# Kernel optimization log

Hardware: AMD Instinct MI355X
Metric: run time of the kernel (lower is better)

## Reference

```python
import jax, jax.numpy as jnp
import numpy as np

B, N, C, H = 4, 4096, 128, 4


def setup_inputs() -> dict:
    key = jax.random.key(0)
    ks = jax.random.split(key, 12)
    def rn(k, shape, s=0.02):
        return jax.random.normal(k, shape, jnp.float32) * s
    return dict(
        x=jax.random.normal(ks[0], (B, N, C), jnp.float32),
        p=jax.random.normal(ks[1], (B, N, 3), jnp.float32),
        fcl1_w=rn(ks[2], (C, C)), fcl1_b=jnp.zeros((C,), jnp.float32),
        # per-head (stacked over leading H axis) TransformerLayer params
        hq_w=rn(ks[3], (H, C, C)), hq_b=jnp.zeros((H, C), jnp.float32),
        hk_w=rn(ks[4], (H, C, C)), hk_b=jnp.zeros((H, C), jnp.float32),
        hv_w=rn(ks[5], (H, C, C)), hv_b=jnp.zeros((H, C), jnp.float32),
        pe1_w=rn(ks[6], (H, C, 3)), pe1_b=jnp.zeros((H, C), jnp.float32),  # Conv1d(3->C, k=1)
        pe2_w=rn(ks[7], (H, C, C)), pe2_b=jnp.zeros((H, C), jnp.float32),  # Conv1d(C->C, k=1)
        mh_w=rn(ks[8], (C, 4 * C)), mh_b=jnp.zeros((C,), jnp.float32),
        fcl2_w=rn(ks[9], (C, C)), fcl2_b=jnp.zeros((C,), jnp.float32),
    )


def reference(x, p, fcl1_w, fcl1_b, hq_w, hq_b, hk_w, hk_b, hv_w, hv_b,
              pe1_w, pe1_b, pe2_w, pe2_b, mh_w, mh_b, fcl2_w, fcl2_b):
    residual = x
    xf = x @ fcl1_w.T + fcl1_b  # fcl1
    scale = 1.0 / jnp.sqrt(jnp.asarray(C, jnp.float32))

    def head(qw, qb, kw, kb, vw, vb, p1w, p1b, p2w, p2b):
        # kernel-size-1 Conv1d == pointwise linear over coords
        pe = jax.nn.relu(jnp.einsum('bnd,cd->bnc', p, p1w) + p1b)
        pe = jnp.einsum('bnc,dc->bnd', pe, p2w) + p2b
        xh = xf + pe
        q = xh @ kw.T + kb  # note: original uses self.key for x_query
        k = xh @ qw.T + qb  # and self.query for x_key (name swap, kept faithful)
        v = xh @ vw.T + vb
        s = jax.nn.softmax(jnp.einsum('bnc,bmc->bnm', q, k) * scale, axis=-1)
        return jnp.einsum('bnm,bmc->bnc', s, v)

    outs = jax.vmap(head)(hq_w, hq_b, hk_w, hk_b, hv_w, hv_b,
                          pe1_w, pe1_b, pe2_w, pe2_b)  # [H,B,N,C]
    cat = jnp.moveaxis(outs, 0, 2).reshape(B, N, H * C)  # concat head1..head4 on last dim
    y = cat @ mh_w.T + mh_b
    y = y @ fcl2_w.T + fcl2_b
    mu = jnp.mean(y, axis=-1, keepdims=True)
    var = jnp.var(y, axis=-1, keepdims=True)
    y = (y - mu) / jnp.sqrt(var + 1e-5)  # torch.layer_norm, no affine
    return (y + residual, p)
```

## Files before the change

kernel.cpp:

```cpp
#include <hip/hip_runtime.h>
#include <hip/hip_bf16.h>

typedef __bf16 bf16;
typedef bf16 bf16x8 __attribute__((ext_vector_type(8)));
typedef float f32x4 __attribute__((ext_vector_type(4)));

static __device__ __forceinline__ f32x4 mfma16(bf16x8 a, bf16x8 b, f32x4 c) {
  return __builtin_amdgcn_mfma_f32_16x16x32_bf16(a, b, c, 0, 0, 0);
}

#define N_SEG 18
#define TOTAL_CONV 2511616

__global__ void probe_k(const unsigned short* __restrict__ xr, int* __restrict__ flag) {
  int wild = 0;
#pragma unroll
  for (int i = 0; i < 8; i++) {
    unsigned short w = xr[threadIdx.x * 8 + i];
    int e = (w >> 7) & 0xFF;
    if (e < 110 || e > 134) wild++;
  }
#pragma unroll
  for (int off = 1; off < 64; off <<= 1) wild += __shfl_xor(wild, off);
  if (threadIdx.x == 0) *flag = (wild > 64) ? 1 : 0;
}

struct ConvArgs { const void* src[N_SEG]; };

__global__ __launch_bounds__(256) void convall_k(ConvArgs a, bf16* __restrict__ dst,
                                                 void* __restrict__ outp,
                                                 const int* __restrict__ flag) {
  const int ends[N_SEG] = {2097152, 2146304, 2162688, 2162816, 2228352, 2228864,
                           2294400, 2294912, 2360448, 2360960, 2362496, 2363008,
                           2428544, 2429056, 2494592, 2495104, 2511488, 2511616};
  int i = blockIdx.x * 256 + threadIdx.x;
  if (i >= TOTAL_CONV) {
    int j = i - TOTAL_CONV;
    if (j < 49152) {
      if (*flag) ((float*)outp)[2097152 + j] = ((const float*)a.src[1])[j];
      else       ((bf16*)outp)[2097152 + j]  = ((const bf16*)a.src[1])[j];
    }
    return;
  }
  int s = 0;
  while (i >= ends[s]) s++;
  int j = i - (s ? ends[s - 1] : 0);
  if (*flag) dst[i] = (bf16)((const float*)a.src[s])[j];
  else       dst[i] = ((const bf16*)a.src[s])[j];
}

__global__ __launch_bounds__(256, 2) void pre_k(
    const bf16* __restrict__ x, const bf16* __restrict__ p,
    const bf16* __restrict__ f1w, const bf16* __restrict__ f1b,
    const bf16* __restrict__ pe1w, const bf16* __restrict__ pe1b,
    const bf16* __restrict__ pe2w, const bf16* __restrict__ pe2b,
    const bf16* __restrict__ Wq, const bf16* __restrict__ Bq,
    const bf16* __restrict__ Wk, const bf16* __restrict__ Bk,
    const bf16* __restrict__ Wv, const bf16* __restrict__ Bv,
    bf16* __restrict__ qo, bf16* __restrict__ ko, bf16* __restrict__ vo)
{
  const int lane = threadIdx.x & 63;
  const int wave = threadIdx.x >> 6;
  const int quad = lane >> 4;
  const int n15 = lane & 15;
  const int h = blockIdx.y;
  const int r0 = blockIdx.x * 64;
  const int wr = wave * 16;

  __shared__ bf16 tile[9216];

  f32x4 acc[8];
  const f32x4 zz = {};

  {
    bf16x8 ap = {};
    if (quad == 0) {
      const bf16* pr = p + (long)(r0 + wr + n15) * 3;
      ap[0] = pr[0]; ap[1] = pr[1]; ap[2] = pr[2];
    }
#pragma unroll
    for (int ct = 0; ct < 8; ct++) {
      bf16x8 bw = {};
      if (quad == 0) {
        const bf16* wp = pe1w + ((long)h * 128 + ct * 16 + n15) * 3;
        bw[0] = wp[0]; bw[1] = wp[1]; bw[2] = wp[2];
      }
      acc[ct] = mfma16(ap, bw, zz);
    }
#pragma unroll
    for (int ct = 0; ct < 8; ct++) {
      const int col = ct * 16 + n15;
      const float bb = (float)pe1b[h * 128 + col];
#pragma unroll
      for (int r = 0; r < 4; r++)
        tile[(wr + quad * 4 + r) * 136 + col] = (bf16)fmaxf(acc[ct][r] + bb, 0.f);
    }
  }

#pragma unroll
  for (int ct = 0; ct < 8; ct++) acc[ct] = zz;
#pragma unroll
  for (int kk = 0; kk < 4; kk++) {
    const int ka = kk * 32 + quad * 8;
    bf16x8 a0 = *(const bf16x8*)&tile[(wr + n15) * 136 + ka];
#pragma unroll
    for (int ct = 0; ct < 8; ct++) {
      bf16x8 wf = *(const bf16x8*)(pe2w + (long)h * 16384 + (long)(ct * 16 + n15) * 128 + ka);
      acc[ct] = mfma16(a0, wf, acc[ct]);
    }
  }
#pragma unroll
  for (int kk = 0; kk < 4; kk++) {
    const int ka = kk * 32 + quad * 8;
    bf16x8 a0 = *(const bf16x8*)(x + (long)(r0 + wr + n15) * 128 + ka);
#pragma unroll
    for (int ct = 0; ct < 8; ct++) {
      bf16x8 wf = *(const bf16x8*)(f1w + (long)(ct * 16 + n15) * 128 + ka);
      acc[ct] = mfma16(a0, wf, acc[ct]);
    }
  }
#pragma unroll
  for (int ct = 0; ct < 8; ct++) {
    const int col = ct * 16 + n15;
    const float bv = (float)pe2b[h * 128 + col] + (float)f1b[col];
#pragma unroll
    for (int r = 0; r < 4; r++)
      tile[(wr + quad * 4 + r) * 136 + col] = (bf16)(acc[ct][r] + bv);
  }

  bf16x8 af[4];
#pragma unroll
  for (int kk = 0; kk < 4; kk++)
    af[kk] = *(const bf16x8*)&tile[(wr + n15) * 136 + kk * 32 + quad * 8];

#pragma unroll
  for (int m = 0; m < 2; m++) {
    f32x4 a2[8];
#pragma unroll
    for (int ct = 0; ct < 8; ct++) a2[ct] = zz;
    const bf16* Wm = (m == 0) ? Wq : Wk;
#pragma unroll
    for (int kk = 0; kk < 4; kk++) {
      const int ka = kk * 32 + quad * 8;
#pragma unroll
      for (int ct = 0; ct < 8; ct++) {
        bf16x8 wf = *(const bf16x8*)(Wm + (long)h * 16384 + (long)(ct * 16 + n15) * 128 + ka);
        a2[ct] = mfma16(af[kk], wf, a2[ct]);
      }
    }
    bf16* oz = ((m == 0) ? qo : ko) + (long)h * 2097152;
    const bf16* Bz = (m == 0) ? Bq : Bk;
#pragma unroll
    for (int ct = 0; ct < 8; ct++) {
      const int col = ct * 16 + n15;
      const float bv = (float)Bz[h * 128 + col];
#pragma unroll
      for (int r = 0; r < 4; r++)
        oz[(long)(r0 + wr + quad * 4 + r) * 128 + col] = (bf16)(a2[ct][r] + bv);
    }
  }

  {
    f32x4 a2[8];
#pragma unroll
    for (int ct = 0; ct < 8; ct++) a2[ct] = zz;
#pragma unroll
    for (int kk = 0; kk < 4; kk++) {
      const int ka = kk * 32 + quad * 8;
#pragma unroll
      for (int ct = 0; ct < 8; ct++) {
        bf16x8 wf = *(const bf16x8*)(Wv + (long)h * 16384 + (long)(ct * 16 + n15) * 128 + ka);
        a2[ct] = mfma16(af[kk], wf, a2[ct]);
      }
    }
    __syncthreads();
#pragma unroll
    for (int ct = 0; ct < 8; ct++) {
      const int col = ct * 16 + n15;
      const float bv = (float)Bv[h * 128 + col];
#pragma unroll
      for (int r = 0; r < 4; r++)
        tile[col * 72 + (wr + quad * 4 + r)] = (bf16)(a2[ct][r] + bv);
    }
    __syncthreads();
    bf16* vz = vo + (long)h * 2097152;
#pragma unroll
    for (int i = 0; i < 16; i++) {
      const int c = wave * 32 + i * 2 + (lane >> 5);
      const int m2 = (lane & 31) * 2;
      *(unsigned int*)&vz[(long)c * 16384 + r0 + m2] =
          *(const unsigned int*)&tile[c * 72 + m2];
    }
  }
}

__global__ __launch_bounds__(256, 2) void attn_k(
    const bf16* __restrict__ Q, const bf16* __restrict__ Kg,
    const bf16* __restrict__ vT, bf16* __restrict__ Op, float* __restrict__ ls)
{
  const int lane = threadIdx.x & 63;
  const int wave = threadIdx.x >> 6;
  const int quad = lane >> 4;
  const int n15 = lane & 15;
  const int qt = blockIdx.x >> 1;
  const int half = blockIdx.x & 1;
  const int b = blockIdx.y, h = blockIdx.z;
  const long qkBase = ((long)h * 4 + b) * 4096 * 128;
  const long vBase = (long)h * (128L * 16384) + (long)b * 4096;
  const int wrow = qt * 128 + wave * 32;
  const int kvStart = half * 2048;

  __shared__ bf16 Kt[64 * 128];
  __shared__ bf16 Vt[128 * 64];
  __shared__ bf16 Pt[4][1024];

  const float scale = 0.08838834764831845f;
  bf16x8 qf[2][4];
#pragma unroll
  for (int g = 0; g < 2; g++)
#pragma unroll
    for (int kk = 0; kk < 4; kk++) {
      bf16x8 t = *(const bf16x8*)(Q + qkBase + (long)(wrow + g * 16 + n15) * 128 + kk * 32 + quad * 8);
#pragma unroll
      for (int j = 0; j < 8; j++) t[j] = (bf16)((float)t[j] * scale);
      qf[g][kk] = t;
    }

  f32x4 Om[2][8] = {};
  float l_part[2][4] = {};

  for (int kv0 = kvStart; kv0 < kvStart + 2048; kv0 += 64) {
    __syncthreads();
    {
      const int rr = threadIdx.x >> 4;
      const int ch = threadIdx.x & 15;
#pragma unroll
      for (int i = 0; i < 4; i++) {
        const int row = rr + i * 16;
        *(bf16x8*)&Kt[row * 128 + ((ch ^ rr) * 8)] =
            *(const bf16x8*)(Kg + qkBase + (long)(kv0 + row) * 128 + ch * 8);
      }
      const int vc = threadIdx.x >> 3;
      const int vch = threadIdx.x & 7;
#pragma unroll
      for (int i = 0; i < 4; i++) {
        const int c = vc + i * 32;
        *(bf16x8*)&Vt[c * 64 + ((vch ^ (c & 7)) * 8)] =
            *(const bf16x8*)(vT + vBase + (long)c * 16384 + kv0 + vch * 8);
      }
    }
    __syncthreads();

    f32x4 S[2][4] = {};
#pragma unroll
    for (int kk = 0; kk < 4; kk++) {
#pragma unroll
      for (int ct = 0; ct < 4; ct++) {
        bf16x8 kf = *(const bf16x8*)&Kt[(ct * 16 + n15) * 128 + (((kk * 4 + quad) ^ n15) * 8)];
        S[0][ct] = mfma16(qf[0][kk], kf, S[0][ct]);
        S[1][ct] = mfma16(qf[1][kk], kf, S[1][ct]);
      }
    }

    bf16x8 pf[2][2];
#pragma unroll
    for (int g = 0; g < 2; g++) {
#pragma unroll
      for (int ct = 0; ct < 4; ct++)
#pragma unroll
        for (int r = 0; r < 4; r++) {
          float e = __expf(S[g][ct][r]);
          l_part[g][r] += e;
          const int row = quad * 4 + r;
          const int kv = ct * 16 + n15;
          Pt[wave][row * 64 + ((((kv >> 3) ^ (row & 7)) * 8)) + (kv & 7)] = (bf16)e;
        }
#pragma unroll
      for (int kk = 0; kk < 2; kk++)
        pf[g][kk] = *(const bf16x8*)&Pt[wave][n15 * 64 + (((kk * 4 + quad) ^ (n15 & 7)) * 8)];
    }

#pragma unroll
    for (int kk = 0; kk < 2; kk++) {
      bf16x8 vf[8];
#pragma unroll
      for (int ct = 0; ct < 8; ct++) {
        const int c = ct * 16 + n15;
        vf[ct] = *(const bf16x8*)&Vt[c * 64 + (((kk * 4 + quad) ^ (c & 7)) * 8)];
      }
#pragma unroll
      for (int g = 0; g < 2; g++)
#pragma unroll
        for (int ct = 0; ct < 8; ct++)
          Om[g][ct] = mfma16(pf[g][kk], vf[ct], Om[g][ct]);
    }
  }

#pragma unroll
  for (int g = 0; g < 2; g++) {
#pragma unroll
    for (int r = 0; r < 4; r++) {
      float s = l_part[g][r];
#pragma unroll
      for (int off = 1; off < 16; off <<= 1) s += __shfl_xor(s, off);
      if (n15 == 0)
        ls[((long)half * 4 + h) * 16384 + b * 4096 + wrow + g * 16 + quad * 4 + r] = s;
    }
    const long ob = (long)half * 8388608 + (long)(b * 4096 + wrow + g * 16 + quad * 4) * 512 + h * 128;
#pragma unroll
    for (int ct = 0; ct < 8; ct++)
#pragma unroll
      for (int r = 0; r < 4; r++)
        Op[ob + (long)r * 512 + ct * 16 + n15] = (bf16)Om[g][ct][r];
  }
}

__global__ __launch_bounds__(256) void tail_k(
    const bf16* __restrict__ Op, const float* __restrict__ ls,
    const bf16* __restrict__ mhw, const bf16* __restrict__ mhb,
    const bf16* __restrict__ f2w, const bf16* __restrict__ f2b,
    const void* __restrict__ xraw, void* __restrict__ outraw,
    const int* __restrict__ flag)
{
  const int lane = threadIdx.x & 63;
  const int wave = threadIdx.x >> 6;
  const int quad = lane >> 4;
  const int n15 = lane & 15;
  const int r0 = blockIdx.x * 64 + wave * 16;
  __shared__ bf16 y1t[64][136];

  float invA[4];
#pragma unroll
  for (int hh = 0; hh < 4; hh++) {
    const float l0 = ls[(long)hh * 16384 + r0 + n15];
    const float l1 = ls[(long)(4 + hh) * 16384 + r0 + n15];
    invA[hh] = 1.f / (l0 + l1);
  }

  f32x4 acc[8] = {};
  for (int k0 = 0; k0 < 512; k0 += 32) {
    const int hh = k0 >> 7;
    const int ka = k0 + quad * 8;
    bf16x8 v0 = *(const bf16x8*)(Op + (long)(r0 + n15) * 512 + ka);
    bf16x8 v1 = *(const bf16x8*)(Op + 8388608L + (long)(r0 + n15) * 512 + ka);
    bf16x8 a0;
#pragma unroll
    for (int j = 0; j < 8; j++)
      a0[j] = (bf16)(((float)v0[j] + (float)v1[j]) * invA[hh]);
#pragma unroll
    for (int ct = 0; ct < 8; ct++) {
      bf16x8 wf = *(const bf16x8*)(mhw + (long)(ct * 16 + n15) * 512 + ka);
      acc[ct] = mfma16(a0, wf, acc[ct]);
    }
  }
#pragma unroll
  for (int ct = 0; ct < 8; ct++) {
    const float bv = (float)mhb[ct * 16 + n15];
#pragma unroll
    for (int r = 0; r < 4; r++)
      y1t[wave * 16 + quad * 4 + r][ct * 16 + n15] = (bf16)(acc[ct][r] + bv);
  }

  f32x4 acc2[8] = {};
  for (int k0 = 0; k0 < 128; k0 += 32) {
    const int ka = k0 + quad * 8;
    bf16x8 a0 = *(const bf16x8*)&y1t[wave * 16 + n15][ka];
#pragma unroll
    for (int ct = 0; ct < 8; ct++) {
      bf16x8 wf = *(const bf16x8*)(f2w + (long)(ct * 16 + n15) * 128 + ka);
      acc2[ct] = mfma16(a0, wf, acc2[ct]);
    }
  }

  float s1[4] = {}, s2[4] = {};
#pragma unroll
  for (int ct = 0; ct < 8; ct++) {
    const float bv = (float)f2b[ct * 16 + n15];
#pragma unroll
    for (int r = 0; r < 4; r++) {
      const float v = acc2[ct][r] + bv;
      acc2[ct][r] = v;
      s1[r] += v;
      s2[r] += v * v;
    }
  }
  float mu[4], inv[4];
#pragma unroll
  for (int r = 0; r < 4; r++) {
    float a = s1[r], b2 = s2[r];
#pragma unroll
    for (int off = 1; off < 16; off <<= 1) {
      a += __shfl_xor(a, off);
      b2 += __shfl_xor(b2, off);
    }
    mu[r] = a * (1.f / 128.f);
    const float var = fmaxf(b2 * (1.f / 128.f) - mu[r] * mu[r], 0.f);
    inv[r] = rsqrtf(var + 1e-5f);
  }

  const int isF32 = *flag;
#pragma unroll
  for (int ct = 0; ct < 8; ct++)
#pragma unroll
    for (int r = 0; r < 4; r++) {
      const long idx = (long)(r0 + quad * 4 + r) * 128 + ct * 16 + n15;
      const float resid = isF32 ? ((const float*)xraw)[idx]
                                : (float)((const bf16*)xraw)[idx];
      const float v = (acc2[ct][r] - mu[r]) * inv[r] + resid;
      if (isF32) ((float*)outraw)[idx] = v;
      else       ((bf16*)outraw)[idx] = (bf16)v;
    }
}

extern "C" void kernel_launch(void* const* d_in, const int* in_sizes, int n_in,
                              void* d_out, int out_size, void* d_ws, size_t ws_size,
                              hipStream_t stream)
{
  bf16* ws  = (bf16*)d_ws;
  bf16* q   = ws;
  bf16* kb  = ws + 8388608;
  bf16* vt  = ws + 16777216;
  bf16* Op  = ws + 25165824;
  float* lsb = (float*)(ws + 41943040);
  const long AR = 42205184;
  int* flag = (int*)(ws + 44720000);

  static const int counts[N_SEG] = {2097152, 49152, 16384, 128, 65536, 512, 65536, 512,
                                    65536, 512, 1536, 512, 65536, 512, 65536, 512, 16384, 128};
  long offs[N_SEG]; long o = AR;
  for (int i = 0; i < N_SEG; i++) { offs[i] = o; o += counts[i]; }
  bf16* xc    = ws + offs[0];
  bf16* pc    = ws + offs[1];
  bf16* f1w   = ws + offs[2];
  bf16* f1b   = ws + offs[3];
  bf16* hqw   = ws + offs[4];
  bf16* hqb   = ws + offs[5];
  bf16* hkw   = ws + offs[6];
  bf16* hkb   = ws + offs[7];
  bf16* hvw   = ws + offs[8];
  bf16* hvb   = ws + offs[9];
  bf16* pe1w  = ws + offs[10];
  bf16* pe1b  = ws + offs[11];
  bf16* pe2w  = ws + offs[12];
  bf16* pe2b  = ws + offs[13];
  bf16* mhw   = ws + offs[14];
  bf16* mhb   = ws + offs[15];
  bf16* f2w   = ws + offs[16];
  bf16* f2b   = ws + offs[17];

  probe_k<<<dim3(1), dim3(64), 0, stream>>>((const unsigned short*)d_in[0], flag);
  ConvArgs ca;
  for (int i = 0; i < N_SEG; i++) ca.src[i] = d_in[i];
  convall_k<<<dim3((TOTAL_CONV + 49152 + 255) / 256), dim3(256), 0, stream>>>(ca, ws + AR, d_out, flag);

  dim3 blk(256);
  pre_k<<<dim3(256, 4), blk, 0, stream>>>(xc, pc, f1w, f1b, pe1w, pe1b, pe2w, pe2b,
                                          hkw, hkb, hqw, hqb, hvw, hvb, q, kb, vt);
  attn_k<<<dim3(64, 4, 4), blk, 0, stream>>>(q, kb, vt, Op, lsb);
  tail_k<<<dim3(256), blk, 0, stream>>>(Op, lsb, mhw, mhb, f2w, f2b, d_in[0], d_out, flag);
}
```

Baseline: 368.9 us.

## Fold softmax scale into Q projection and stream Q fragments from global in attention loop

Moves the 1/sqrt(C) scale into the Q projection epilogue so the attention kernel no longer rescales Q. The attention kernel stops holding the Q fragments in registers and reloads them from global memory (through the cache) on every KV tile. It also gives each 16-row group its own P buffer in shared memory so P fragments are loaded just before their use. The aim is to cut register pressure, which may help occupancy under launch_bounds(256,2), at the cost of repeated global Q loads and doubled Pt shared memory.

```diff
diff --git a/kernel.cpp b/kernel.cpp
--- a/kernel.cpp
+++ b/kernel.cpp
@@ -150,13 +150,14 @@
     }
     bf16* oz = ((m == 0) ? qo : ko) + (long)h * 2097152;
     const bf16* Bz = (m == 0) ? Bq : Bk;
+    const float sc = (m == 0) ? 0.08838834764831845f : 1.0f;
 #pragma unroll
     for (int ct = 0; ct < 8; ct++) {
       const int col = ct * 16 + n15;
       const float bv = (float)Bz[h * 128 + col];
 #pragma unroll
       for (int r = 0; r < 4; r++)
-        oz[(long)(r0 + wr + quad * 4 + r) * 128 + col] = (bf16)(a2[ct][r] + bv);
+        oz[(long)(r0 + wr + quad * 4 + r) * 128 + col] = (bf16)((a2[ct][r] + bv) * sc);
     }
   }
 
@@ -212,19 +213,9 @@
 
   __shared__ bf16 Kt[64 * 128];
   __shared__ bf16 Vt[128 * 64];
-  __shared__ bf16 Pt[4][1024];
-
-  const float scale = 0.08838834764831845f;
-  bf16x8 qf[2][4];
-#pragma unroll
-  for (int g = 0; g < 2; g++)
-#pragma unroll
-    for (int kk = 0; kk < 4; kk++) {
-      bf16x8 t = *(const bf16x8*)(Q + qkBase + (long)(wrow + g * 16 + n15) * 128 + kk * 32 + quad * 8);
-#pragma unroll
-      for (int j = 0; j < 8; j++) t[j] = (bf16)((float)t[j] * scale);
-      qf[g][kk] = t;
-    }
+  __shared__ bf16 Pt[8][1024];
+
+  const bf16* qrow = Q + qkBase + (long)(wrow + n15) * 128 + quad * 8;
 
   f32x4 Om[2][8] = {};
   float l_part[2][4] = {};
@@ -254,17 +245,18 @@
     f32x4 S[2][4] = {};
 #pragma unroll
     for (int kk = 0; kk < 4; kk++) {
+      bf16x8 q0 = *(const bf16x8*)(qrow + kk * 32);
+      bf16x8 q1 = *(const bf16x8*)(qrow + 2048 + kk * 32);
 #pragma unroll
       for (int ct = 0; ct < 4; ct++) {
         bf16x8 kf = *(const bf16x8*)&Kt[(ct * 16 + n15) * 128 + (((kk * 4 + quad) ^ n15) * 8)];
-        S[0][ct] = mfma16(qf[0][kk], kf, S[0][ct]);
-        S[1][ct] = mfma16(qf[1][kk], kf, S[1][ct]);
-      }
-    }
-
-    bf16x8 pf[2][2];
-#pragma unroll
-    for (int g = 0; g < 2; g++) {
+        S[0][ct] = mfma16(q0, kf, S[0][ct]);
+        S[1][ct] = mfma16(q1, kf, S[1][ct]);
+      }
+    }
+
+#pragma unroll
+    for (int g = 0; g < 2; g++)
 #pragma unroll
       for (int ct = 0; ct < 4; ct++)
 #pragma unroll
@@ -273,12 +265,8 @@
           l_part[g][r] += e;
           const int row = quad * 4 + r;
           const int kv = ct * 16 + n15;
-          Pt[wave][row * 64 + ((((kv >> 3) ^ (row & 7)) * 8)) + (kv & 7)] = (bf16)e;
+          Pt[wave * 2 + g][row * 64 + ((((kv >> 3) ^ (row & 7)) * 8)) + (kv & 7)] = (bf16)e;
         }
-#pragma unroll
-      for (int kk = 0; kk < 2; kk++)
-        pf[g][kk] = *(const bf16x8*)&Pt[wave][n15 * 64 + (((kk * 4 + quad) ^ (n15 & 7)) * 8)];
-    }
 
 #pragma unroll
     for (int kk = 0; kk < 2; kk++) {
@@ -289,10 +277,12 @@
         vf[ct] = *(const bf16x8*)&Vt[c * 64 + (((kk * 4 + quad) ^ (c & 7)) * 8)];
       }
 #pragma unroll
-      for (int g = 0; g < 2; g++)
+      for (int g = 0; g < 2; g++) {
+        bf16x8 pf = *(const bf16x8*)&Pt[wave * 2 + g][n15 * 64 + (((kk * 4 + quad) ^ (n15 & 7)) * 8)];
 #pragma unroll
         for (int ct = 0; ct < 8; ct++)
-          Om[g][ct] = mfma16(pf[g][kk], vf[ct], Om[g][ct]);
+          Om[g][ct] = mfma16(pf, vf[ct], Om[g][ct]);
+      }
     }
   }
 
```

Measured after the change: 367.2 us. Within noise of the previous version (-0.5%).
